# Kernel optimization log

Measured on AMD Instinct MI355X. Metric: run time of the kernel, lower is better.

Reference implementation:

```python
import jax, jax.numpy as jnp
import numpy as np

B, D, G, C = 4096, 512, 128, 10
THR = 0.95          # reliability_threshold
LR_MAX, LR_MIN = 0.2, 0.05
CTX_MAX, CTX_MIN = 2, 0


def setup_inputs() -> dict:
    key = jax.random.key(0)
    k1, k2, k3, k4, k5 = jax.random.split(key, 5)
    activations = jax.random.uniform(k1, (B, D), jnp.float32)
    labels = jax.random.randint(k2, (B,), 0, C)
    som_vectors = jax.random.uniform(k3, (G, G, D), jnp.float32) * 0.5 + 0.5
    cell_labels = jax.random.randint(k4, (G, G), 0, C)
    cell_reliability = jax.random.uniform(k5, (G, G), jnp.float32) * 100.0
    return dict(activations=activations, labels=labels, som_vectors=som_vectors,
                cell_labels=cell_labels, cell_reliability=cell_reliability,
                epoch=10, max_epochs=100)


def reference(activations, labels, som_vectors, cell_labels, cell_reliability, epoch, max_epochs):
    # --- schedule (static python scalars) ---
    progress = (max_epochs - epoch) / max_epochs if max_epochs > 0 else 0
    progress = max(0.0, min(1.0, progress))
    som_context = CTX_MIN + int(progress ** 4 * (CTX_MAX - CTX_MIN))
    som_lr = LR_MIN + progress * (LR_MAX - LR_MIN)

    flat_som = som_vectors.reshape(-1, D)                 # (N, D), N = G*G
    # --- squared-euclidean distance matrix (B, N) ---
    x_norm = jnp.sum(activations ** 2, axis=1, keepdims=True)
    w_norm = jnp.sum(flat_som ** 2, axis=1)[None, :]
    dists = jnp.clip(x_norm + w_norm - 2.0 * activations @ flat_som.T, 0.0, None)
    min_dists = jnp.min(dists, axis=1)
    bmu = jnp.argmin(dists, axis=1)                        # (B,)

    # --- class-constrained BMU for SOM error ---
    flat_labels = cell_labels.reshape(-1)
    label_mask = flat_labels[None, :] != labels[:, None]   # (B, N)
    class_dists = jnp.where(label_mask, jnp.inf, dists)
    class_bmu = jnp.argmin(class_dists, axis=1)
    class_bmu_vectors = flat_som[class_bmu]                # (B, D)
    rel = cell_reliability.reshape(-1)[class_bmu] / 100.0  # (B,)
    valid = (rel >= THR).astype(activations.dtype)
    som_errors = 0.01 * rel[:, None] * (class_bmu_vectors - activations) * valid[:, None]

    # --- batch neighborhood SOM update (matches torch code, incl. x/y convention) ---
    bmu_x = bmu // G
    bmu_y = bmu % G
    coords = jnp.arange(G)
    dist_y = jnp.abs(coords[None, :] - bmu_y[:, None])     # (B, G) rows (y_grid) vs bmu_y
    dist_x = jnp.abs(coords[None, :] - bmu_x[:, None])     # (B, G) cols (x_grid) vs bmu_x
    cheb = jnp.maximum(dist_y[:, :, None], dist_x[:, None, :])   # (B, G, G)
    powers = (som_lr / 2.0 ** cheb.astype(activations.dtype)) * (cheb <= som_context)
    denom = powers.sum(axis=0)[..., None]                  # (G, G, 1)
    numerator = jnp.einsum('bn,bd->nd', powers.reshape(B, -1), activations).reshape(G, G, D)
    updated = som_vectors + numerator - som_vectors * denom
    new_som = jnp.where(jnp.mean(min_dists) > 1e-4, updated, som_vectors)

    return som_errors, new_som
```

## Files before the change

kernel.cpp:

```cpp
#include <hip/hip_runtime.h>
#include <math.h>

#define B_ 4096
#define D_ 512
#define G_ 128
#define N_ (G_*G_)
#define NTP 64
#define THR_ 0.95f
#define IMAX_ 0x7FFFFFFF

typedef float f32x4 __attribute__((ext_vector_type(4)));
typedef _Float16 half8 __attribute__((ext_vector_type(8)));

__global__ __launch_bounds__(256) void split_hi_kernel(const float* __restrict__ src,
                                                       _Float16* __restrict__ hi, int n4) {
    int i = blockIdx.x * 256 + threadIdx.x;
    if (i >= n4) return;
    float4 v = ((const float4*)src)[i];
    float vv[4] = {v.x, v.y, v.z, v.w};
    union { _Float16 h[4]; uint64_t u64; } H;
    #pragma unroll
    for (int j = 0; j < 4; j++) H.h[j] = (_Float16)vv[j];
    ((uint64_t*)hi)[i] = H.u64;
}

__global__ __launch_bounds__(256) void prep_w_kernel(const float* __restrict__ W,
                                                     _Float16* __restrict__ hi,
                                                     float* __restrict__ wnorm) {
    int n = blockIdx.x * 4 + (threadIdx.x >> 6);
    int t = threadIdx.x & 63;
    const float* row = W + (size_t)n * D_;
    float4 a = ((const float4*)row)[t];
    float4 b = ((const float4*)row)[t + 64];
    float av[4] = {a.x, a.y, a.z, a.w}, bv[4] = {b.x, b.y, b.z, b.w};
    union { _Float16 h[4]; uint64_t u64; } Ha, Hb;
    #pragma unroll
    for (int j = 0; j < 4; j++) { Ha.h[j] = (_Float16)av[j]; Hb.h[j] = (_Float16)bv[j]; }
    ((uint64_t*)(hi + (size_t)n * D_))[t]       = Ha.u64;
    ((uint64_t*)(hi + (size_t)n * D_ + 256))[t] = Hb.u64;
    float s = a.x*a.x + a.y*a.y + a.z*a.z + a.w*a.w
            + b.x*b.x + b.y*b.y + b.z*b.z + b.w*b.w;
    #pragma unroll
    for (int off = 32; off > 0; off >>= 1) s += __shfl_down(s, off, 64);
    if (t == 0) wnorm[n] = s;
}

__device__ __forceinline__ unsigned long long packmin(float v, int n) {
    unsigned u = __float_as_uint(v);
    u ^= (u & 0x80000000u) ? 0xFFFFFFFFu : 0x80000000u;
    return ((unsigned long long)u << 32) | (unsigned)n;
}
__device__ __forceinline__ void unpackmin(unsigned long long pkt, float* v, int* n) {
    unsigned u = (unsigned)(pkt >> 32);
    u = (u & 0x80000000u) ? (u ^ 0x80000000u) : ~u;
    *v = __uint_as_float(u);
    *n = (int)(unsigned)pkt;
}


#define PH_WAIT_(N) asm volatile("s_waitcnt vmcnt(" #N ")" ::: "memory")
#define PH_WAIT(N) PH_WAIT_(N)
#define WAITLGKM0 asm volatile("s_waitcnt lgkmcnt(0)" ::: "memory")
#define SBAR __builtin_amdgcn_s_barrier()
#define SCHED0 __builtin_amdgcn_sched_barrier(0)
#define PRIO1 __builtin_amdgcn_s_setprio(1)
#define PRIO0 __builtin_amdgcn_s_setprio(0)

#define STAGE_HALF(GBASE, LOFF, TAU, H) do { \
    __builtin_amdgcn_global_load_lds( \
        (const __attribute__((address_space(1))) void*)((GBASE) + (size_t)(H) * (128 * D_) + (TAU) * 64 + srcoff0), \
        (__attribute__((address_space(3))) void*)(smem + (LOFF) + (((TAU) & 1) << 15) + ((H) << 14) + ldsoff0), 16, 0, 0); \
    __builtin_amdgcn_global_load_lds( \
        (const __attribute__((address_space(1))) void*)((GBASE) + (size_t)(H) * (128 * D_) + (TAU) * 64 + srcoff1), \
        (__attribute__((address_space(3))) void*)(smem + (LOFF) + (((TAU) & 1) << 15) + ((H) << 14) + ldsoff1), 16, 0, 0); \
} while (0)

#define TILE(TAU, S1, S3, S4, DO_W, VM4) do { \
    half8 af[4][2], bl[2][2], bh[2][2]; \
     \
    _Pragma("unroll") for (int mi = 0; mi < 4; mi++) { \
        af[mi][0] = *(const half8*)(smem + (((TAU) & 1) << 15) + sA + mi * 2048 + swz0); \
        af[mi][1] = *(const half8*)(smem + (((TAU) & 1) << 15) + sA + mi * 2048 + swz1); } \
    _Pragma("unroll") for (int ni = 0; ni < 2; ni++) { \
        bl[ni][0] = *(const half8*)(smem + 65536 + (((TAU) & 1) << 15) + sB + ni * 2048 + swz0); \
        bl[ni][1] = *(const half8*)(smem + 65536 + (((TAU) & 1) << 15) + sB + ni * 2048 + swz1); } \
    if (S1) STAGE_HALF(Abase, 0, (TAU) + 1, 1); \
    SBAR; WAITLGKM0; SCHED0; PRIO1; \
    _Pragma("unroll") for (int mi = 0; mi < 4; mi++) \
      _Pragma("unroll") for (int ni = 0; ni < 2; ni++) { \
        acc[mi][ni] = __builtin_amdgcn_mfma_f32_16x16x32_f16(af[mi][0], bl[ni][0], acc[mi][ni], 0, 0, 0); \
        acc[mi][ni] = __builtin_amdgcn_mfma_f32_16x16x32_f16(af[mi][1], bl[ni][1], acc[mi][ni], 0, 0, 0); } \
    PRIO0; SCHED0; SBAR; \
     \
    _Pragma("unroll") for (int ni = 0; ni < 2; ni++) { \
        bh[ni][0] = *(const half8*)(smem + 65536 + (((TAU) & 1) << 15) + sB + (ni + 2) * 2048 + swz0); \
        bh[ni][1] = *(const half8*)(smem + 65536 + (((TAU) & 1) << 15) + sB + (ni + 2) * 2048 + swz1); } \
    SBAR; WAITLGKM0; SCHED0; PRIO1; \
    _Pragma("unroll") for (int mi = 0; mi < 4; mi++) \
      _Pragma("unroll") for (int ni = 0; ni < 2; ni++) { \
        acc[mi][ni + 2] = __builtin_amdgcn_mfma_f32_16x16x32_f16(af[mi][0], bh[ni][0], acc[mi][ni + 2], 0, 0, 0); \
        acc[mi][ni + 2] = __builtin_amdgcn_mfma_f32_16x16x32_f16(af[mi][1], bh[ni][1], acc[mi][ni + 2], 0, 0, 0); } \
    PRIO0; SCHED0; SBAR; \
     \
    _Pragma("unroll") for (int mi = 0; mi < 4; mi++) { \
        af[mi][0] = *(const half8*)(smem + (((TAU) & 1) << 15) + sA + (mi + 4) * 2048 + swz0); \
        af[mi][1] = *(const half8*)(smem + (((TAU) & 1) << 15) + sA + (mi + 4) * 2048 + swz1); } \
    if (S3) STAGE_HALF(Wbase, 65536, (TAU) + 2, 0); \
    SBAR; WAITLGKM0; SCHED0; PRIO1; \
    _Pragma("unroll") for (int mi = 0; mi < 4; mi++) \
      _Pragma("unroll") for (int ni = 0; ni < 2; ni++) { \
        acc[mi + 4][ni + 2] = __builtin_amdgcn_mfma_f32_16x16x32_f16(af[mi][0], bh[ni][0], acc[mi + 4][ni + 2], 0, 0, 0); \
        acc[mi + 4][ni + 2] = __builtin_amdgcn_mfma_f32_16x16x32_f16(af[mi][1], bh[ni][1], acc[mi + 4][ni + 2], 0, 0, 0); } \
    PRIO0; SCHED0; SBAR; \
     \
    if (S4) { STAGE_HALF(Abase, 0, (TAU) + 2, 0); STAGE_HALF(Wbase, 65536, (TAU) + 2, 1); } \
    if (DO_W) PH_WAIT(VM4); \
    SBAR; PRIO1; \
    _Pragma("unroll") for (int mi = 0; mi < 4; mi++) \
      _Pragma("unroll") for (int ni = 0; ni < 2; ni++) { \
        acc[mi + 4][ni] = __builtin_amdgcn_mfma_f32_16x16x32_f16(af[mi][0], bl[ni][0], acc[mi + 4][ni], 0, 0, 0); \
        acc[mi + 4][ni] = __builtin_amdgcn_mfma_f32_16x16x32_f16(af[mi][1], bl[ni][1], acc[mi + 4][ni], 0, 0, 0); } \
    PRIO0; SCHED0; SBAR; \
} while (0)

__global__ __launch_bounds__(512, 2) void score_mfma_kernel(
    const _Float16* __restrict__ Ah, const _Float16* __restrict__ Wh,
    const float* __restrict__ wnorm,
    const int* __restrict__ labels, const int* __restrict__ clabels,
    float* __restrict__ pminv, int* __restrict__ pmini,
    float* __restrict__ pcminv, int* __restrict__ pcmini)
{
    __shared__ __align__(16) char smem[131072];

    const int tid  = threadIdx.x;
    const int lane = tid & 63;
    const int wave = tid >> 6;
    const int wm = wave >> 2, wn = wave & 3;
    const int c = lane & 15, quad = lane >> 4;

    const int o = blockIdx.x;
    const int xcd = o & 7, idx = o >> 3;
    const int ntile = (xcd << 3) | (idx & 7);
    const int mtile = idx >> 3;
    const int m0 = mtile * 256, n0 = ntile * 256;

    const _Float16* Abase = Ah + (size_t)m0 * D_;
    const _Float16* Wbase = Wh + (size_t)n0 * D_;

    const int i0 = tid, i1 = 512 + tid;
    const int rl0 = i0 >> 3, sl0 = i0 & 7, rl1 = i1 >> 3, sl1 = i1 & 7;
    const size_t srcoff0 = (size_t)rl0 * D_ + ((sl0 ^ (rl0 & 7)) << 3);
    const size_t srcoff1 = (size_t)rl1 * D_ + ((sl1 ^ (rl1 & 7)) << 3);
    const int ldsoff0 = i0 << 4, ldsoff1 = i1 << 4;

    const int sA = (wm * 128 + c) * 128;
    const int sB = (wn * 64 + c) * 128;
    const int swz0 = ((0 * 4 + quad) ^ (c & 7)) << 4;
    const int swz1 = ((1 * 4 + quad) ^ (c & 7)) << 4;

    f32x4 acc[8][4];
    #pragma unroll
    for (int i = 0; i < 8; i++)
        #pragma unroll
        for (int j = 0; j < 4; j++)
            acc[i][j] = (f32x4){0.f, 0.f, 0.f, 0.f};

    STAGE_HALF(Abase, 0, 0, 0);
    STAGE_HALF(Wbase, 65536, 0, 0);
    STAGE_HALF(Wbase, 65536, 0, 1);
    STAGE_HALF(Abase, 0, 0, 1);
    STAGE_HALF(Abase, 0, 1, 0);
    STAGE_HALF(Wbase, 65536, 1, 0);
    STAGE_HALF(Wbase, 65536, 1, 1);
    PH_WAIT(6); SBAR;

    TILE(0, 1, 1, 1, 1, 6);
    TILE(1, 1, 1, 1, 1, 6);
    TILE(2, 1, 1, 1, 1, 6);
    TILE(3, 1, 1, 1, 1, 6);
    TILE(4, 1, 1, 1, 1, 6);
    TILE(5, 1, 1, 1, 1, 6);
    TILE(6, 1, 0, 0, 1, 0);
    TILE(7, 0, 0, 0, 0, 0);

    __syncthreads();

    const unsigned long long ID = (0xFF800000ull << 32) | 0x7FFFFFFFull;
    float wnl[4]; int cll[4];
    #pragma unroll
    for (int ni = 0; ni < 4; ni++) {
        int n = n0 + wn * 64 + ni * 16 + c;
        wnl[ni] = wnorm[n];
        cll[ni] = clabels[n];
    }

    unsigned long long (*tbl)[64] = (unsigned long long (*)[64])smem;
    unsigned long long cbst[8][4];

    #pragma unroll
    for (int mi = 0; mi < 8; mi++) {
        #pragma unroll
        for (int r = 0; r < 4; r++) {
            int rowl = wm * 128 + mi * 16 + quad * 4 + r;
            int lb = labels[m0 + rowl];
            unsigned long long bb = ID, cb = ID;
            #pragma unroll
            for (int ni = 0; ni < 4; ni++) {
                float s = fmaf(-2.f, acc[mi][ni][r], wnl[ni]);
                unsigned long long pk = packmin(s, n0 + wn * 64 + ni * 16 + c);
                bb = bb < pk ? bb : pk;
                if (cll[ni] == lb) cb = cb < pk ? cb : pk;
            }
            tbl[rowl][(wn * 16 + c) ^ (rowl & 15)] = bb;
            cbst[mi][r] = cb;
        }
    }
    __syncthreads();
    if (tid < 256) {
        int row = tid;
        unsigned long long m = ID;
        #pragma unroll
        for (int j = 0; j < 64; j++) {
            unsigned long long v = tbl[row][j ^ (row & 15)];
            m = m < v ? m : v;
        }
        float v; int n; unpackmin(m, &v, &n);
        size_t pp = (size_t)(m0 + row) * NTP + ntile;
        pminv[pp] = v; pmini[pp] = n;
    }
    __syncthreads();
    #pragma unroll
    for (int mi = 0; mi < 8; mi++)
        #pragma unroll
        for (int r = 0; r < 4; r++) {
            int rowl = wm * 128 + mi * 16 + quad * 4 + r;
            tbl[rowl][(wn * 16 + c) ^ (rowl & 15)] = cbst[mi][r];
        }
    __syncthreads();
    if (tid < 256) {
        int row = tid;
        unsigned long long m = ID;
        #pragma unroll
        for (int j = 0; j < 64; j++) {
            unsigned long long v = tbl[row][j ^ (row & 15)];
            m = m < v ? m : v;
        }
        float v; int n; unpackmin(m, &v, &n);
        size_t pp = (size_t)(m0 + row) * NTP + ntile;
        pcminv[pp] = v; pcmini[pp] = n;
    }
}

__global__ __launch_bounds__(128) void reduce_kernel(
    const float* __restrict__ A, const float* __restrict__ W,
    const float* __restrict__ crel,
    const float* __restrict__ pminv, const int* __restrict__ pmini,
    const float* __restrict__ pcminv, const int* __restrict__ pcmini,
    int* __restrict__ bmu, float* __restrict__ sum_min, float* __restrict__ out0,
    float* __restrict__ S, float* __restrict__ count)
{
    int b = blockIdx.x, t = threadIdx.x;
    __shared__ float sv[128]; __shared__ int si[128];
    __shared__ float scv[128]; __shared__ int sci[128];
    __shared__ float xs[128];
    __shared__ int   cbmu_s;

    {
        float4 z = {0.f, 0.f, 0.f, 0.f};
        #pragma unroll
        for (int k = 0; k < 4; k++)
            ((float4*)S)[((size_t)(b * 4 + k)) * 128 + t] = z;
        if (t < 4) count[b * 4 + t] = 0.f;
    }

    if (t < NTP) {
        size_t p = (size_t)b * NTP + t;
        sv[t] = pminv[p]; si[t] = pmini[p]; scv[t] = pcminv[p]; sci[t] = pcmini[p];
    } else {
        sv[t] = INFINITY; si[t] = IMAX_; scv[t] = INFINITY; sci[t] = IMAX_;
    }

    float4 x4 = ((const float4*)(A + (size_t)b * D_))[t];
    xs[t] = x4.x*x4.x + x4.y*x4.y + x4.z*x4.z + x4.w*x4.w;
    __syncthreads();
    for (int s = 64; s > 0; s >>= 1) {
        if (t < s) {
            float v = sv[t+s]; int idx = si[t+s];
            if (v < sv[t] || (v == sv[t] && idx < si[t])) { sv[t] = v; si[t] = idx; }
            v = scv[t+s]; idx = sci[t+s];
            if (v < scv[t] || (v == scv[t] && idx < sci[t])) { scv[t] = v; sci[t] = idx; }
            xs[t] += xs[t+s];
        }
        __syncthreads();
    }
    if (t == 0) {
        bmu[b] = si[0];
        float md = xs[0] + sv[0];
        if (md < 0.f) md = 0.f;
        atomicAdd(&sum_min[b & 63], md);
        cbmu_s = sci[0];
    }
    __syncthreads();
    int cb = cbmu_s;
    float r = crel[cb] / 100.0f;
    float val = (r >= THR_) ? 1.0f : 0.0f;
    float sc = 0.01f * r * val;
    float4 w4 = ((const float4*)(W + (size_t)cb * D_))[t];
    float4 o;
    o.x = sc * (w4.x - x4.x); o.y = sc * (w4.y - x4.y);
    o.z = sc * (w4.z - x4.z); o.w = sc * (w4.w - x4.w);
    ((float4*)(out0 + (size_t)b * D_))[t] = o;
}

__global__ __launch_bounds__(512) void scatter1_kernel(
    const float* __restrict__ A, const int* __restrict__ bmu,
    float* S, float* count, float* __restrict__ sum_min)
{
    int b = blockIdx.x, d = threadIdx.x;
    if (b == 0 && d == 0) {
        float s = 0.f;
        for (int i = 0; i < 64; i++) s += sum_min[i];
        sum_min[64] = s;
    }
    int bm = bmu[b];
    float x = A[(size_t)b * D_ + d];
    atomicAdd(&S[(size_t)bm * D_ + d], x);
    if (d == 0) atomicAdd(&count[bm], 1.0f);
}

__global__ __launch_bounds__(256) void final_kernel(
    const float* __restrict__ som, const float* __restrict__ S,
    const float* __restrict__ count, const float* __restrict__ sum_min,
    const int* __restrict__ epoch_p, const int* __restrict__ maxep_p,
    float* __restrict__ out1)
{
    size_t i4 = (size_t)blockIdx.x * 256 + threadIdx.x;
    if (i4 >= (size_t)N_ * D_ / 4) return;
    int n = (int)(i4 >> 7);
    int d4 = (int)(i4 & 127);
    float4 s = ((const float4*)som)[i4];
    bool gate = sum_min[64] > 1e-4f * (float)B_;
    float4 o = s;
    if (gate) {
        int ep = epoch_p[0], me = maxep_p[0];
        float progress = (me > 0) ? (float)(me - ep) / (float)me : 0.f;
        progress = fminf(fmaxf(progress, 0.f), 1.f);
        float p2 = progress * progress;
        int ctx = (int)(p2 * p2 * 2.0f);
        float lr = 0.05f + progress * 0.15f;

        int i = n / G_, j = n % G_;
        float4 nu = {0.f, 0.f, 0.f, 0.f};
        float dn = 0.f;
        for (int di = -ctx; di <= ctx; di++) {
            int ia = i - di; if (ia < 0 || ia >= G_) continue;
            for (int dj = -ctx; dj <= ctx; dj++) {
                int jb = j - dj; if (jb < 0 || jb >= G_) continue;
                int ad = abs(di), aj = abs(dj);
                int cheb = ad > aj ? ad : aj;
                float coef = ldexpf(lr, -cheb);
                float4 t4 = ((const float4*)S)[(size_t)(jb * G_ + ia) * 128 + d4];
                nu.x += coef * t4.x; nu.y += coef * t4.y;
                nu.z += coef * t4.z; nu.w += coef * t4.w;
                dn += coef * count[jb * G_ + ia];
            }
        }
        o.x = s.x + nu.x - s.x * dn;
        o.y = s.y + nu.y - s.y * dn;
        o.z = s.z + nu.z - s.z * dn;
        o.w = s.w + nu.w - s.w * dn;
    }
    ((float4*)out1)[i4] = o;
}

extern "C" void kernel_launch(void* const* d_in, const int* in_sizes, int n_in,
                              void* d_out, int out_size, void* d_ws, size_t ws_size,
                              hipStream_t stream) {
    const float* A   = (const float*)d_in[0];
    const int*   lab = (const int*)d_in[1];
    const float* W   = (const float*)d_in[2];
    const int*   cl  = (const int*)d_in[3];
    const float* cr  = (const float*)d_in[4];
    const int*   ep  = (const int*)d_in[5];
    const int*   me  = (const int*)d_in[6];

    float* out0 = (float*)d_out;
    float* out1 = out0 + (size_t)B_ * D_;

    const size_t MB = 1024 * 1024;
    uint8_t* w = (uint8_t*)d_ws;
    _Float16* Ahi  = (_Float16*)(w);
    _Float16* Whi  = (_Float16*)(w + 4 * MB);
    float* S       = (float*)(w);
    float* pminv   = (float*)(w + 32 * MB);
    int*   pmini   = (int*)  (w + 34 * MB);
    float* pcminv  = (float*)(w + 36 * MB);
    int*   pcmini  = (int*)  (w + 38 * MB);
    float* wnorm   = (float*)(w + 40 * MB);
    float* count   = (float*)(w + 40 * MB + 128 * 1024);
    int*   bmu     = (int*)  (w + 40 * MB + 192 * 1024);
    float* sum_min = (float*)(w + 40 * MB + 256 * 1024);

    hipMemsetAsync(sum_min, 0, 65 * sizeof(float), stream);

    split_hi_kernel<<<(B_ * D_ / 4 + 255) / 256, 256, 0, stream>>>(A, Ahi, B_ * D_ / 4);
    prep_w_kernel<<<N_ / 4, 256, 0, stream>>>(W, Whi, wnorm);

    score_mfma_kernel<<<dim3((B_ / 256) * (N_ / 256)), 512, 0, stream>>>(
        Ahi, Whi, wnorm, lab, cl, pminv, pmini, pcminv, pcmini);

    reduce_kernel<<<B_, 128, 0, stream>>>(A, W, cr, pminv, pmini, pcminv, pcmini,
                                          bmu, sum_min, out0, S, count);

    scatter1_kernel<<<B_, 512, 0, stream>>>(A, bmu, S, count, sum_min);

    final_kernel<<<(N_ * D_ / 4 + 255) / 256, 256, 0, stream>>>(
        W, S, count, sum_min, ep, me, out1);
}
```

Before: 275.8 us.

## Merge prep kernels and memset, fuse scatter into reduce when workspace allows

Folds the fp16 split of A, the W prep with norms, the sum_min memset and the zeroing of count and S into one prep kernel. When the workspace is large enough, S gets its own region so the atomic scatter of activations into S moves into reduce_kernel and the separate scatter launch is dropped. The final kernel now sums the partial min-distances itself. This removes launches and a pass that rereads A, but zeroing 32MB of S in the prep kernel adds write traffic, and the fused path only runs if ws_size is at least 80MB.

```diff
diff --git a/kernel.cpp b/kernel.cpp
--- a/kernel.cpp
+++ b/kernel.cpp
@@ -12,37 +12,48 @@
 typedef float f32x4 __attribute__((ext_vector_type(4)));
 typedef _Float16 half8 __attribute__((ext_vector_type(8)));
 
-__global__ __launch_bounds__(256) void split_hi_kernel(const float* __restrict__ src,
-                                                       _Float16* __restrict__ hi, int n4) {
-    int i = blockIdx.x * 256 + threadIdx.x;
-    if (i >= n4) return;
-    float4 v = ((const float4*)src)[i];
-    float vv[4] = {v.x, v.y, v.z, v.w};
-    union { _Float16 h[4]; uint64_t u64; } H;
-    #pragma unroll
-    for (int j = 0; j < 4; j++) H.h[j] = (_Float16)vv[j];
-    ((uint64_t*)hi)[i] = H.u64;
-}
-
-__global__ __launch_bounds__(256) void prep_w_kernel(const float* __restrict__ W,
-                                                     _Float16* __restrict__ hi,
-                                                     float* __restrict__ wnorm) {
-    int n = blockIdx.x * 4 + (threadIdx.x >> 6);
-    int t = threadIdx.x & 63;
-    const float* row = W + (size_t)n * D_;
-    float4 a = ((const float4*)row)[t];
-    float4 b = ((const float4*)row)[t + 64];
-    float av[4] = {a.x, a.y, a.z, a.w}, bv[4] = {b.x, b.y, b.z, b.w};
-    union { _Float16 h[4]; uint64_t u64; } Ha, Hb;
-    #pragma unroll
-    for (int j = 0; j < 4; j++) { Ha.h[j] = (_Float16)av[j]; Hb.h[j] = (_Float16)bv[j]; }
-    ((uint64_t*)(hi + (size_t)n * D_))[t]       = Ha.u64;
-    ((uint64_t*)(hi + (size_t)n * D_ + 256))[t] = Hb.u64;
-    float s = a.x*a.x + a.y*a.y + a.z*a.z + a.w*a.w
-            + b.x*b.x + b.y*b.y + b.z*b.z + b.w*b.w;
-    #pragma unroll
-    for (int off = 32; off > 0; off >>= 1) s += __shfl_down(s, off, 64);
-    if (t == 0) wnorm[n] = s;
+__global__ __launch_bounds__(256) void prep_kernel(
+    const float* __restrict__ A, const float* __restrict__ W,
+    _Float16* __restrict__ Ahi, _Float16* __restrict__ Whi,
+    float* __restrict__ wnorm, float* __restrict__ S,
+    float* __restrict__ count, float* __restrict__ sum_min)
+{
+    const int blk = blockIdx.x, tid = threadIdx.x;
+    if (blk < 2048) {
+        int i = blk * 256 + tid;
+        float4 v = ((const float4*)A)[i];
+        float vv[4] = {v.x, v.y, v.z, v.w};
+        union { _Float16 h[4]; uint64_t u64; } H;
+        #pragma unroll
+        for (int j = 0; j < 4; j++) H.h[j] = (_Float16)vv[j];
+        ((uint64_t*)Ahi)[i] = H.u64;
+    } else if (blk < 6144) {
+        int n = (blk - 2048) * 4 + (tid >> 6);
+        int t = tid & 63;
+        const float* row = W + (size_t)n * D_;
+        float4 a = ((const float4*)row)[t];
+        float4 b = ((const float4*)row)[t + 64];
+        float av[4] = {a.x, a.y, a.z, a.w}, bv[4] = {b.x, b.y, b.z, b.w};
+        union { _Float16 h[4]; uint64_t u64; } Ha, Hb;
+        #pragma unroll
+        for (int j = 0; j < 4; j++) { Ha.h[j] = (_Float16)av[j]; Hb.h[j] = (_Float16)bv[j]; }
+        ((uint64_t*)(Whi + (size_t)n * D_))[t]       = Ha.u64;
+        ((uint64_t*)(Whi + (size_t)n * D_ + 256))[t] = Hb.u64;
+        float s = a.x*a.x + a.y*a.y + a.z*a.z + a.w*a.w
+                + b.x*b.x + b.y*b.y + b.z*b.z + b.w*b.w;
+        #pragma unroll
+        for (int off = 32; off > 0; off >>= 1) s += __shfl_down(s, off, 64);
+        if (t == 0) wnorm[n] = s;
+    } else if (blk < 6160) {
+        if (blk == 6144 && tid < 65) sum_min[tid] = 0.f;
+        int j = (blk - 6144) * 256 + tid;
+        float4 z = {0.f, 0.f, 0.f, 0.f};
+        ((float4*)count)[j] = z;
+    } else {
+        size_t i = (size_t)(blk - 6160) * 256 + tid;
+        float4 z = {0.f, 0.f, 0.f, 0.f};
+        ((float4*)S)[i] = z;
+    }
 }
 
 __device__ __forceinline__ unsigned long long packmin(float v, int n) {
@@ -77,7 +88,6 @@
 
 #define TILE(TAU, S1, S3, S4, DO_W, VM4) do { \
     half8 af[4][2], bl[2][2], bh[2][2]; \
-     \
     _Pragma("unroll") for (int mi = 0; mi < 4; mi++) { \
         af[mi][0] = *(const half8*)(smem + (((TAU) & 1) << 15) + sA + mi * 2048 + swz0); \
         af[mi][1] = *(const half8*)(smem + (((TAU) & 1) << 15) + sA + mi * 2048 + swz1); } \
@@ -91,7 +101,6 @@
         acc[mi][ni] = __builtin_amdgcn_mfma_f32_16x16x32_f16(af[mi][0], bl[ni][0], acc[mi][ni], 0, 0, 0); \
         acc[mi][ni] = __builtin_amdgcn_mfma_f32_16x16x32_f16(af[mi][1], bl[ni][1], acc[mi][ni], 0, 0, 0); } \
     PRIO0; SCHED0; SBAR; \
-     \
     _Pragma("unroll") for (int ni = 0; ni < 2; ni++) { \
         bh[ni][0] = *(const half8*)(smem + 65536 + (((TAU) & 1) << 15) + sB + (ni + 2) * 2048 + swz0); \
         bh[ni][1] = *(const half8*)(smem + 65536 + (((TAU) & 1) << 15) + sB + (ni + 2) * 2048 + swz1); } \
@@ -101,7 +110,6 @@
         acc[mi][ni + 2] = __builtin_amdgcn_mfma_f32_16x16x32_f16(af[mi][0], bh[ni][0], acc[mi][ni + 2], 0, 0, 0); \
         acc[mi][ni + 2] = __builtin_amdgcn_mfma_f32_16x16x32_f16(af[mi][1], bh[ni][1], acc[mi][ni + 2], 0, 0, 0); } \
     PRIO0; SCHED0; SBAR; \
-     \
     _Pragma("unroll") for (int mi = 0; mi < 4; mi++) { \
         af[mi][0] = *(const half8*)(smem + (((TAU) & 1) << 15) + sA + (mi + 4) * 2048 + swz0); \
         af[mi][1] = *(const half8*)(smem + (((TAU) & 1) << 15) + sA + (mi + 4) * 2048 + swz1); } \
@@ -112,7 +120,6 @@
         acc[mi + 4][ni + 2] = __builtin_amdgcn_mfma_f32_16x16x32_f16(af[mi][0], bh[ni][0], acc[mi + 4][ni + 2], 0, 0, 0); \
         acc[mi + 4][ni + 2] = __builtin_amdgcn_mfma_f32_16x16x32_f16(af[mi][1], bh[ni][1], acc[mi + 4][ni + 2], 0, 0, 0); } \
     PRIO0; SCHED0; SBAR; \
-     \
     if (S4) { STAGE_HALF(Abase, 0, (TAU) + 2, 0); STAGE_HALF(Wbase, 65536, (TAU) + 2, 1); } \
     if (DO_W) PH_WAIT(VM4); \
     SBAR; PRIO1; \
@@ -257,7 +264,7 @@
     const float* __restrict__ pminv, const int* __restrict__ pmini,
     const float* __restrict__ pcminv, const int* __restrict__ pcmini,
     int* __restrict__ bmu, float* __restrict__ sum_min, float* __restrict__ out0,
-    float* __restrict__ S, float* __restrict__ count)
+    float* __restrict__ S, float* __restrict__ count, int fused)
 {
     int b = blockIdx.x, t = threadIdx.x;
     __shared__ float sv[128]; __shared__ int si[128];
@@ -265,12 +272,11 @@
     __shared__ float xs[128];
     __shared__ int   cbmu_s;
 
-    {
+    if (!fused) {
         float4 z = {0.f, 0.f, 0.f, 0.f};
         #pragma unroll
         for (int k = 0; k < 4; k++)
             ((float4*)S)[((size_t)(b * 4 + k)) * 128 + t] = z;
-        if (t < 4) count[b * 4 + t] = 0.f;
     }
 
     if (t < NTP) {
@@ -310,18 +316,21 @@
     o.x = sc * (w4.x - x4.x); o.y = sc * (w4.y - x4.y);
     o.z = sc * (w4.z - x4.z); o.w = sc * (w4.w - x4.w);
     ((float4*)(out0 + (size_t)b * D_))[t] = o;
+
+    if (fused) {
+        int bm = si[0];
+        float* Sr = S + (size_t)bm * D_ + t * 4;
+        atomicAdd(&Sr[0], x4.x); atomicAdd(&Sr[1], x4.y);
+        atomicAdd(&Sr[2], x4.z); atomicAdd(&Sr[3], x4.w);
+        if (t == 0) atomicAdd(&count[bm], 1.0f);
+    }
 }
 
 __global__ __launch_bounds__(512) void scatter1_kernel(
     const float* __restrict__ A, const int* __restrict__ bmu,
-    float* S, float* count, float* __restrict__ sum_min)
+    float* S, float* count)
 {
     int b = blockIdx.x, d = threadIdx.x;
-    if (b == 0 && d == 0) {
-        float s = 0.f;
-        for (int i = 0; i < 64; i++) s += sum_min[i];
-        sum_min[64] = s;
-    }
     int bm = bmu[b];
     float x = A[(size_t)b * D_ + d];
     atomicAdd(&S[(size_t)bm * D_ + d], x);
@@ -334,12 +343,19 @@
     const int* __restrict__ epoch_p, const int* __restrict__ maxep_p,
     float* __restrict__ out1)
 {
+    __shared__ float gsum;
+    if (threadIdx.x == 0) {
+        float s = 0.f;
+        for (int i = 0; i < 64; i++) s += sum_min[i];
+        gsum = s;
+    }
+    __syncthreads();
+
     size_t i4 = (size_t)blockIdx.x * 256 + threadIdx.x;
-    if (i4 >= (size_t)N_ * D_ / 4) return;
     int n = (int)(i4 >> 7);
     int d4 = (int)(i4 & 127);
     float4 s = ((const float4*)som)[i4];
-    bool gate = sum_min[64] > 1e-4f * (float)B_;
+    bool gate = gsum > 1e-4f * (float)B_;
     float4 o = s;
     if (gate) {
         int ep = epoch_p[0], me = maxep_p[0];
@@ -391,7 +407,6 @@
     uint8_t* w = (uint8_t*)d_ws;
     _Float16* Ahi  = (_Float16*)(w);
     _Float16* Whi  = (_Float16*)(w + 4 * MB);
-    float* S       = (float*)(w);
     float* pminv   = (float*)(w + 32 * MB);
     int*   pmini   = (int*)  (w + 34 * MB);
     float* pcminv  = (float*)(w + 36 * MB);
@@ -401,19 +416,21 @@
     int*   bmu     = (int*)  (w + 40 * MB + 192 * 1024);
     float* sum_min = (float*)(w + 40 * MB + 256 * 1024);
 
-    hipMemsetAsync(sum_min, 0, 65 * sizeof(float), stream);
-
-    split_hi_kernel<<<(B_ * D_ / 4 + 255) / 256, 256, 0, stream>>>(A, Ahi, B_ * D_ / 4);
-    prep_w_kernel<<<N_ / 4, 256, 0, stream>>>(W, Whi, wnorm);
+    const int fused = (ws_size >= 80 * MB) ? 1 : 0;
+    float* S = fused ? (float*)(w + 48 * MB) : (float*)w;
+
+    prep_kernel<<<fused ? 14352 : 6160, 256, 0, stream>>>(
+        A, W, Ahi, Whi, wnorm, S, count, sum_min);
 
     score_mfma_kernel<<<dim3((B_ / 256) * (N_ / 256)), 512, 0, stream>>>(
         Ahi, Whi, wnorm, lab, cl, pminv, pmini, pcminv, pcmini);
 
     reduce_kernel<<<B_, 128, 0, stream>>>(A, W, cr, pminv, pmini, pcminv, pcmini,
-                                          bmu, sum_min, out0, S, count);
-
-    scatter1_kernel<<<B_, 512, 0, stream>>>(A, bmu, S, count, sum_min);
-
-    final_kernel<<<(N_ * D_ / 4 + 255) / 256, 256, 0, stream>>>(
+                                          bmu, sum_min, out0, S, count, fused);
+
+    if (!fused)
+        scatter1_kernel<<<B_, 512, 0, stream>>>(A, bmu, S, count);
+
+    final_kernel<<<(N_ * D_ / 4) / 256, 256, 0, stream>>>(
         W, S, count, sum_min, ep, me, out1);
 }
```

After: 326.8 us. 1.18x slower.
